# Performance work log

Measured on AMD Instinct MI355X. Metric: run time of the kernel, lower is better.

Reference implementation:

```python
import jax, jax.numpy as jnp
import numpy as np

N_NODES = 100000
N_EDGES = 4000000
CHANNELS = 64


def setup_inputs() -> dict:
    key = jax.random.key(0)
    k1, k2, k3, k4, k5 = jax.random.split(key, 5)
    x = jax.random.normal(k1, (N_NODES, CHANNELS), dtype=jnp.float32)
    sources = jax.random.randint(k2, (N_EDGES,), 0, N_NODES, dtype=jnp.int64)
    targets = jax.random.randint(k3, (N_EDGES,), 0, N_NODES, dtype=jnp.int64)
    norm = jax.random.uniform(k4, (N_NODES, 1), dtype=jnp.float32)
    # xavier_normal_ for a (64, 64) weight: std = sqrt(2 / (fan_in + fan_out))
    std = float(np.sqrt(2.0 / (CHANNELS + CHANNELS)))
    weight = jax.random.normal(k5, (CHANNELS, CHANNELS), dtype=jnp.float32) * std
    return {"x": x, "sources": sources, "targets": targets, "norm": norm, "weight": weight}


def reference(x, sources, targets, norm, weight):
    # x.index_add(0, targets, x[sources]) == x + segment_sum(x[sources], targets)
    messages = x[sources]  # [E, C] gather
    agg = x + jax.ops.segment_sum(messages, targets, num_segments=x.shape[0])  # [N, C]
    h = norm * agg  # per-node scale, norm broadcasts [N,1] over [N,C]
    return h @ weight  # [N, C]
```

## Files before the change

kernel.cpp:

```cpp
#include <hip/hip_runtime.h>


constexpr int C = 64;
constexpr int BN = 128;
constexpr int CHUNK2 = 8192;
constexpr int MAXB = 1024;
constexpr int NPASS = 3;
constexpr int BINS = BN * 4;
constexpr int ASTRIDE = 65;
constexpr int UNI = BN * ASTRIDE;
constexpr int TAILCAP = 65536;

__global__ __launch_bounds__(256) void init_kernel(
    int* __restrict__ cursor, int* __restrict__ tailcnt, int NB, int slot) {
  int i = blockIdx.x * 256 + threadIdx.x;
  if (i < NB) cursor[i] = i * slot;
  if (i == NB) *tailcnt = 0;
}

__global__ __launch_bounds__(512) void binfused_kernel(
    const int* __restrict__ src, const int* __restrict__ tgt,
    int* __restrict__ gcursor, int* __restrict__ tailcnt,
    unsigned* __restrict__ tailrec, unsigned* __restrict__ recs,
    const float* __restrict__ x, unsigned* __restrict__ xb,
    int E, int NB, int slot, int binBlocks, int total8) {
  if ((int)blockIdx.x >= binBlocks) {
    int i = (blockIdx.x - binBlocks) * 512 + threadIdx.x;
    if (i < total8) {
      const float4* x4 = (const float4*)x;
      float4 a = x4[i * 2], bq = x4[i * 2 + 1];
      float f[8] = {a.x, a.y, a.z, a.w, bq.x, bq.y, bq.z, bq.w};
      unsigned w[4];
#pragma unroll
      for (int k = 0; k < 4; k++) {
        unsigned u0 = __float_as_uint(f[2 * k]);
        unsigned u1 = __float_as_uint(f[2 * k + 1]);
        u0 = (u0 + 0x7FFFu + ((u0 >> 16) & 1u)) >> 16;
        u1 = (u1 + 0x7FFFu + ((u1 >> 16) & 1u)) >> 16;
        w[k] = u0 | (u1 << 16);
      }
      ((uint4*)xb)[i] = make_uint4(w[0], w[1], w[2], w[3]);
    }
    return;
  }
  __shared__ unsigned rec[CHUNK2];
  __shared__ unsigned short bkt[CHUNK2];
  __shared__ int hist[MAXB];
  __shared__ int gb[MAXB];
  int tid = threadIdx.x;
  int base = blockIdx.x * CHUNK2;
  int count = E - base; if (count > CHUNK2) count = CHUNK2;

  for (int i = tid; i < NB; i += 512) hist[i] = 0;
  __syncthreads();
  int nv = count >> 2;
  const int4* s4 = (const int4*)(src + base);
  const int4* t4 = (const int4*)(tgt + base);
  for (int i = tid; i < nv; i += 512) {
    int4 s = s4[i], t = t4[i];
    unsigned r0 = ((unsigned)s.x << 7) | (unsigned)(t.x & 127);
    unsigned r1 = ((unsigned)s.y << 7) | (unsigned)(t.y & 127);
    unsigned r2 = ((unsigned)s.z << 7) | (unsigned)(t.z & 127);
    unsigned r3 = ((unsigned)s.w << 7) | (unsigned)(t.w & 127);
    ((uint4*)rec)[i] = make_uint4(r0, r1, r2, r3);
    int b0 = t.x >> 7, b1 = t.y >> 7, b2 = t.z >> 7, b3 = t.w >> 7;
    ((ushort4*)bkt)[i] = make_ushort4(
        (unsigned short)b0, (unsigned short)b1,
        (unsigned short)b2, (unsigned short)b3);
    atomicAdd(&hist[b0], 1); atomicAdd(&hist[b1], 1);
    atomicAdd(&hist[b2], 1); atomicAdd(&hist[b3], 1);
  }
  for (int i = (nv << 2) + tid; i < count; i += 512) {
    int s = src[base + i], t = tgt[base + i];
    int b = t >> 7;
    rec[i] = ((unsigned)s << 7) | (unsigned)(t & 127);
    bkt[i] = (unsigned short)b;
    atomicAdd(&hist[b], 1);
  }
  __syncthreads();
  for (int i = tid; i < NB; i += 512) {
    int c = hist[i];
    gb[i] = c ? atomicAdd(&gcursor[i], c) : 0;
  }
  __syncthreads();
  for (int i = tid; i < NB; i += 512) hist[i] = 0;
  __syncthreads();
  for (int i = tid; i < count; i += 512) {
    int b = (int)bkt[i];
    int idx = atomicAdd(&hist[b], 1);
    int dest = gb[b] + idx;
    if (dest < (b + 1) * slot) {
      recs[dest] = rec[i];
    } else {
      int tp = atomicAdd(tailcnt, 1);
      if (tp < TAILCAP) {
        tailrec[2 * tp] = rec[i];
        tailrec[2 * tp + 1] = (unsigned)b;
      }
    }
  }
}

__device__ __forceinline__ void acc8_bf16(float (&a)[8], uint4 v) {
  a[0] += __uint_as_float(v.x << 16);
  a[1] += __uint_as_float(v.x & 0xFFFF0000u);
  a[2] += __uint_as_float(v.y << 16);
  a[3] += __uint_as_float(v.y & 0xFFFF0000u);
  a[4] += __uint_as_float(v.z << 16);
  a[5] += __uint_as_float(v.z & 0xFFFF0000u);
  a[6] += __uint_as_float(v.w << 16);
  a[7] += __uint_as_float(v.w & 0xFFFF0000u);
}

__device__ __forceinline__ void acc8_f32(float (&a)[8], float4 u, float4 v) {
  a[0] += u.x; a[1] += u.y; a[2] += u.z; a[3] += u.w;
  a[4] += v.x; a[5] += v.y; a[6] += v.z; a[7] += v.w;
}

template <bool USE_BF16>
__global__ __launch_bounds__(512, 2) void sortgather_kernel(
    const float* __restrict__ x, const unsigned* __restrict__ xb,
    const unsigned* __restrict__ recs, const int* __restrict__ cursor,
    const int* __restrict__ tailcnt, const unsigned* __restrict__ tailrec,
    const float* __restrict__ norm, const float* __restrict__ W,
    float* __restrict__ out, int N, int slot) {
  __shared__ int cnt[BINS];
  __shared__ int pre[BINS];
  __shared__ int nst[BINS + 1];
  __shared__ float uni[UNI];
  unsigned* sorted = (unsigned*)uni;
  float* accum = uni;
  int tid = threadIdx.x;
  int lane = tid & 63;
  int wave = tid >> 6;
  int b = blockIdx.x;
  int n0 = b * BN;
  int nn = N - n0; if (nn > BN) nn = BN;
  int beg = b * slot;
  int m = cursor[b] - beg; if (m > slot) m = slot;
  int end = beg + m;

  float wreg[C];
#pragma unroll
  for (int k = 0; k < C; k++) wreg[k] = W[k * C + lane];

  cnt[tid] = 0;
  __syncthreads();
  for (int r = beg + tid; r < end; r += 512) {
    unsigned rc = recs[r];
    int q = (int)(rc >> 22); if (q > 2) q = 2;
    atomicAdd(&cnt[(int)(rc & 127u) * 4 + q], 1);
  }
  __syncthreads();
  pre[tid] = cnt[tid];
  __syncthreads();
  for (int off = 1; off < BINS; off <<= 1) {
    int v = pre[tid];
    int a = (tid >= off) ? pre[tid - off] : 0;
    __syncthreads();
    pre[tid] = v + a;
    __syncthreads();
  }
  {
    int excl = pre[tid] - cnt[tid];
    nst[tid] = excl;
    cnt[tid] = excl;
  }
  if (tid == 0) nst[BINS] = m;
  __syncthreads();
  for (int r = beg + tid; r < end; r += 512) {
    unsigned rc = recs[r];
    int q = (int)(rc >> 22); if (q > 2) q = 2;
    int p = atomicAdd(&cnt[(int)(rc & 127u) * 4 + q], 1);
    sorted[p] = rc >> 7;
  }
  __syncthreads();

  int l7 = tid & 7;
  int g  = tid >> 3;
  int k0 = g, k1 = g + 64;
  bool has0 = k0 < nn, has1 = k1 < nn;
  const float4* x4 = (const float4*)x;
  const uint4* xb4 = (const uint4*)xb;

  float a0[8], a1[8];
  if (has0) {
    float4 u = x4[(n0 + k0) * 16 + l7 * 2], v = x4[(n0 + k0) * 16 + l7 * 2 + 1];
    a0[0] = u.x; a0[1] = u.y; a0[2] = u.z; a0[3] = u.w;
    a0[4] = v.x; a0[5] = v.y; a0[6] = v.z; a0[7] = v.w;
  } else {
#pragma unroll
    for (int j = 0; j < 8; j++) a0[j] = 0.0f;
  }
  if (has1) {
    float4 u = x4[(n0 + k1) * 16 + l7 * 2], v = x4[(n0 + k1) * 16 + l7 * 2 + 1];
    a1[0] = u.x; a1[1] = u.y; a1[2] = u.z; a1[3] = u.w;
    a1[4] = v.x; a1[5] = v.y; a1[6] = v.z; a1[7] = v.w;
  } else {
#pragma unroll
    for (int j = 0; j < 8; j++) a1[j] = 0.0f;
  }

#pragma unroll
  for (int p = 0; p < NPASS; p++) {
    if (has0) {
      int e = nst[k0 * 4 + p], ge = nst[k0 * 4 + p + 1];
      for (; e + 1 < ge; e += 2) {
        int s0 = (int)sorted[e], s1 = (int)sorted[e + 1];
        if (USE_BF16) {
          uint4 v0 = xb4[s0 * 8 + l7];
          uint4 v1 = xb4[s1 * 8 + l7];
          acc8_bf16(a0, v0); acc8_bf16(a0, v1);
        } else {
          float4 u0 = x4[s0 * 16 + l7 * 2], w0 = x4[s0 * 16 + l7 * 2 + 1];
          float4 u1 = x4[s1 * 16 + l7 * 2], w1 = x4[s1 * 16 + l7 * 2 + 1];
          acc8_f32(a0, u0, w0); acc8_f32(a0, u1, w1);
        }
      }
      if (e < ge) {
        int s = (int)sorted[e];
        if (USE_BF16) { uint4 v = xb4[s * 8 + l7]; acc8_bf16(a0, v); }
        else { acc8_f32(a0, x4[s * 16 + l7 * 2], x4[s * 16 + l7 * 2 + 1]); }
      }
    }
    if (has1) {
      int e = nst[k1 * 4 + p], ge = nst[k1 * 4 + p + 1];
      for (; e + 1 < ge; e += 2) {
        int s0 = (int)sorted[e], s1 = (int)sorted[e + 1];
        if (USE_BF16) {
          uint4 v0 = xb4[s0 * 8 + l7];
          uint4 v1 = xb4[s1 * 8 + l7];
          acc8_bf16(a1, v0); acc8_bf16(a1, v1);
        } else {
          float4 u0 = x4[s0 * 16 + l7 * 2], w0 = x4[s0 * 16 + l7 * 2 + 1];
          float4 u1 = x4[s1 * 16 + l7 * 2], w1 = x4[s1 * 16 + l7 * 2 + 1];
          acc8_f32(a1, u0, w0); acc8_f32(a1, u1, w1);
        }
      }
      if (e < ge) {
        int s = (int)sorted[e];
        if (USE_BF16) { uint4 v = xb4[s * 8 + l7]; acc8_bf16(a1, v); }
        else { acc8_f32(a1, x4[s * 16 + l7 * 2], x4[s * 16 + l7 * 2 + 1]); }
      }
    }
  }

  {
    int tc = *tailcnt; if (tc > TAILCAP) tc = TAILCAP;
    for (int r = 0; r < tc; r++) {
      if ((int)tailrec[2 * r + 1] != b) continue;
      unsigned rc = tailrec[2 * r];
      int tl = (int)(rc & 127u);
      if (tl == k0 || tl == k1) {
        int s = (int)(rc >> 7);
        if (USE_BF16) {
          uint4 v = xb4[s * 8 + l7];
          if (tl == k0) acc8_bf16(a0, v); else acc8_bf16(a1, v);
        } else {
          float4 u = x4[s * 16 + l7 * 2], w = x4[s * 16 + l7 * 2 + 1];
          if (tl == k0) acc8_f32(a0, u, w); else acc8_f32(a1, u, w);
        }
      }
    }
  }
  __syncthreads();

  if (has0) {
#pragma unroll
    for (int j = 0; j < 8; j++) accum[k0 * ASTRIDE + 8 * l7 + j] = a0[j];
  }
  if (has1) {
#pragma unroll
    for (int j = 0; j < 8; j++) accum[k1 * ASTRIDE + 8 * l7 + j] = a1[j];
  }
  __syncthreads();

  for (int i = wave; i < nn; i += 8) {
    int n = n0 + i;
    float a = accum[i * ASTRIDE + lane];
    float o = 0.0f;
#pragma unroll
    for (int c = 0; c < C; c++)
      o = fmaf(__shfl(a, c, 64), wreg[c], o);
    out[n * C + lane] = o * norm[n];
  }
}

extern "C" void kernel_launch(void* const* d_in, const int* in_sizes, int n_in,
                              void* d_out, int out_size, void* d_ws, size_t ws_size,
                              hipStream_t stream) {
  const float* x       = (const float*)d_in[0];
  const int*   sources = (const int*)d_in[1];
  const int*   targets = (const int*)d_in[2];
  const float* norm    = (const float*)d_in[3];
  const float* weight  = (const float*)d_in[4];
  float* out = (float*)d_out;

  int N = in_sizes[0] / C;
  int E = in_sizes[1];
  int NB = (N + BN - 1) / BN;

  size_t availw = ws_size / 4;
  size_t xw = (size_t)N * C / 2;
  size_t fixedw = (size_t)NB + 1 + 2 * (size_t)TAILCAP;
  bool use_bf16; int slot;
  if (availw >= xw + fixedw + (size_t)NB * 8192) { use_bf16 = true; slot = 8192; }
  else if (availw >= xw + fixedw + (size_t)NB * 6144) { use_bf16 = true; slot = 6144; }
  else {
    use_bf16 = false;
    size_t s = (availw > fixedw) ? (availw - fixedw) / (size_t)NB : 0;
    slot = s > 8192 ? 8192 : (int)s;
  }

  unsigned* xb; int* cursor;
  if (use_bf16) {
    xb = (unsigned*)d_ws;
    cursor = (int*)d_ws + xw;
  } else {
    xb = nullptr;
    cursor = (int*)d_ws;
  }
  int* tailcnt = cursor + NB;
  unsigned* tailrec = (unsigned*)(tailcnt + 1);
  unsigned* recs = tailrec + 2 * (size_t)TAILCAP;

  int hb = (E + CHUNK2 - 1) / CHUNK2;
  int total8 = N * C / 8;
  int cvtBlocks = use_bf16 ? (total8 + 511) / 512 : 0;

  init_kernel<<<(NB + 256) / 256, 256, 0, stream>>>(cursor, tailcnt, NB, slot);
  binfused_kernel<<<hb + cvtBlocks, 512, 0, stream>>>(
      sources, targets, cursor, tailcnt, tailrec, recs, x, xb,
      E, NB, slot, hb, total8);
  if (use_bf16) {
    sortgather_kernel<true><<<NB, 512, 0, stream>>>(
        x, xb, recs, cursor, tailcnt, tailrec, norm, weight, out, N, slot);
  } else {
    sortgather_kernel<false><<<NB, 512, 0, stream>>>(
        x, xb, recs, cursor, tailcnt, tailrec, norm, weight, out, N, slot);
  }
}
```

Baseline: 280.5 us.

## Refine source-range passes, cache records in registers, and single-pass binning offsets

In the binning kernel, the local offset returned by the histogram atomic is now kept with the bucket id, so the second atomic pass and the histogram reset go away. In the gather kernel, each thread loads its up to 16 records into registers once instead of reading global memory twice. Source-range sub-bins grow from 4 to 8 per target, giving finer locality across 7 passes; the scan handles two bins per thread. The W register load moves after sorting, the pass loop is no longer unrolled, and the occupancy hint rises to 6. Risks: register pressure from myrec plus wreg, and the code silently assumes at most 8192 records per bucket (slot).

Result: slower. 344.2 us (+22.7%).

```diff
diff --git a/kernel.cpp b/kernel.cpp
--- a/kernel.cpp
+++ b/kernel.cpp
@@ -5,8 +5,8 @@
 constexpr int BN = 128;
 constexpr int CHUNK2 = 8192;
 constexpr int MAXB = 1024;
-constexpr int NPASS = 3;
-constexpr int BINS = BN * 4;
+constexpr int NPASS = 7;
+constexpr int BINS = BN * 8;
 constexpr int ASTRIDE = 65;
 constexpr int UNI = BN * ASTRIDE;
 constexpr int TAILCAP = 65536;
@@ -44,7 +44,7 @@
     return;
   }
   __shared__ unsigned rec[CHUNK2];
-  __shared__ unsigned short bkt[CHUNK2];
+  __shared__ unsigned bi[CHUNK2];
   __shared__ int hist[MAXB];
   __shared__ int gb[MAXB];
   int tid = threadIdx.x;
@@ -64,18 +64,21 @@
     unsigned r3 = ((unsigned)s.w << 7) | (unsigned)(t.w & 127);
     ((uint4*)rec)[i] = make_uint4(r0, r1, r2, r3);
     int b0 = t.x >> 7, b1 = t.y >> 7, b2 = t.z >> 7, b3 = t.w >> 7;
-    ((ushort4*)bkt)[i] = make_ushort4(
-        (unsigned short)b0, (unsigned short)b1,
-        (unsigned short)b2, (unsigned short)b3);
-    atomicAdd(&hist[b0], 1); atomicAdd(&hist[b1], 1);
-    atomicAdd(&hist[b2], 1); atomicAdd(&hist[b3], 1);
+    unsigned i0 = (unsigned)atomicAdd(&hist[b0], 1);
+    unsigned i1 = (unsigned)atomicAdd(&hist[b1], 1);
+    unsigned i2 = (unsigned)atomicAdd(&hist[b2], 1);
+    unsigned i3 = (unsigned)atomicAdd(&hist[b3], 1);
+    ((uint4*)bi)[i] = make_uint4(((unsigned)b0 << 13) | i0,
+                                 ((unsigned)b1 << 13) | i1,
+                                 ((unsigned)b2 << 13) | i2,
+                                 ((unsigned)b3 << 13) | i3);
   }
   for (int i = (nv << 2) + tid; i < count; i += 512) {
     int s = src[base + i], t = tgt[base + i];
     int b = t >> 7;
     rec[i] = ((unsigned)s << 7) | (unsigned)(t & 127);
-    bkt[i] = (unsigned short)b;
-    atomicAdd(&hist[b], 1);
+    unsigned ix = (unsigned)atomicAdd(&hist[b], 1);
+    bi[i] = ((unsigned)b << 13) | ix;
   }
   __syncthreads();
   for (int i = tid; i < NB; i += 512) {
@@ -83,12 +86,10 @@
     gb[i] = c ? atomicAdd(&gcursor[i], c) : 0;
   }
   __syncthreads();
-  for (int i = tid; i < NB; i += 512) hist[i] = 0;
-  __syncthreads();
   for (int i = tid; i < count; i += 512) {
-    int b = (int)bkt[i];
-    int idx = atomicAdd(&hist[b], 1);
-    int dest = gb[b] + idx;
+    unsigned v = bi[i];
+    int b = (int)(v >> 13);
+    int dest = gb[b] + (int)(v & 8191u);
     if (dest < (b + 1) * slot) {
       recs[dest] = rec[i];
     } else {
@@ -118,14 +119,14 @@
 }
 
 template <bool USE_BF16>
-__global__ __launch_bounds__(512, 2) void sortgather_kernel(
+__global__ __launch_bounds__(512, 6) void sortgather_kernel(
     const float* __restrict__ x, const unsigned* __restrict__ xb,
     const unsigned* __restrict__ recs, const int* __restrict__ cursor,
     const int* __restrict__ tailcnt, const unsigned* __restrict__ tailrec,
     const float* __restrict__ norm, const float* __restrict__ W,
     float* __restrict__ out, int N, int slot) {
   __shared__ int cnt[BINS];
-  __shared__ int pre[BINS];
+  __shared__ int pre[512];
   __shared__ int nst[BINS + 1];
   __shared__ float uni[UNI];
   unsigned* sorted = (unsigned*)uni;
@@ -140,21 +141,27 @@
   int m = cursor[b] - beg; if (m > slot) m = slot;
   int end = beg + m;
 
-  float wreg[C];
-#pragma unroll
-  for (int k = 0; k < C; k++) wreg[k] = W[k * C + lane];
-
-  cnt[tid] = 0;
-  __syncthreads();
-  for (int r = beg + tid; r < end; r += 512) {
-    unsigned rc = recs[r];
-    int q = (int)(rc >> 22); if (q > 2) q = 2;
-    atomicAdd(&cnt[(int)(rc & 127u) * 4 + q], 1);
-  }
-  __syncthreads();
-  pre[tid] = cnt[tid];
-  __syncthreads();
-  for (int off = 1; off < BINS; off <<= 1) {
+  unsigned myrec[16];
+#pragma unroll
+  for (int j = 0; j < 16; j++) {
+    int r = beg + tid + j * 512;
+    myrec[j] = (r < end) ? recs[r] : 0xFFFFFFFFu;
+  }
+  cnt[tid] = 0; cnt[tid + 512] = 0;
+  __syncthreads();
+#pragma unroll
+  for (int j = 0; j < 16; j++) {
+    unsigned rc = myrec[j];
+    if (rc != 0xFFFFFFFFu) {
+      int q = (int)(rc >> 21); if (q > 6) q = 6;
+      atomicAdd(&cnt[((int)(rc & 127u) << 3) | q], 1);
+    }
+  }
+  __syncthreads();
+  int c0 = cnt[2 * tid], c1 = cnt[2 * tid + 1];
+  pre[tid] = c0 + c1;
+  __syncthreads();
+  for (int off = 1; off < 512; off <<= 1) {
     int v = pre[tid];
     int a = (tid >= off) ? pre[tid - off] : 0;
     __syncthreads();
@@ -162,19 +169,28 @@
     __syncthreads();
   }
   {
-    int excl = pre[tid] - cnt[tid];
-    nst[tid] = excl;
-    cnt[tid] = excl;
+    int run = pre[tid] - (c0 + c1);
+    nst[2 * tid] = run;
+    nst[2 * tid + 1] = run + c0;
+    cnt[2 * tid] = run;
+    cnt[2 * tid + 1] = run + c0;
   }
   if (tid == 0) nst[BINS] = m;
   __syncthreads();
-  for (int r = beg + tid; r < end; r += 512) {
-    unsigned rc = recs[r];
-    int q = (int)(rc >> 22); if (q > 2) q = 2;
-    int p = atomicAdd(&cnt[(int)(rc & 127u) * 4 + q], 1);
-    sorted[p] = rc >> 7;
-  }
-  __syncthreads();
+#pragma unroll
+  for (int j = 0; j < 16; j++) {
+    unsigned rc = myrec[j];
+    if (rc != 0xFFFFFFFFu) {
+      int q = (int)(rc >> 21); if (q > 6) q = 6;
+      int p = atomicAdd(&cnt[((int)(rc & 127u) << 3) | q], 1);
+      sorted[p] = rc >> 7;
+    }
+  }
+  __syncthreads();
+
+  float wreg[C];
+#pragma unroll
+  for (int k = 0; k < C; k++) wreg[k] = W[k * C + lane];
 
   int l7 = tid & 7;
   int g  = tid >> 3;
@@ -201,10 +217,9 @@
     for (int j = 0; j < 8; j++) a1[j] = 0.0f;
   }
 
-#pragma unroll
   for (int p = 0; p < NPASS; p++) {
     if (has0) {
-      int e = nst[k0 * 4 + p], ge = nst[k0 * 4 + p + 1];
+      int e = nst[k0 * 8 + p], ge = nst[k0 * 8 + p + 1];
       for (; e + 1 < ge; e += 2) {
         int s0 = (int)sorted[e], s1 = (int)sorted[e + 1];
         if (USE_BF16) {
@@ -224,7 +239,7 @@
       }
     }
     if (has1) {
-      int e = nst[k1 * 4 + p], ge = nst[k1 * 4 + p + 1];
+      int e = nst[k1 * 8 + p], ge = nst[k1 * 8 + p + 1];
       for (; e + 1 < ge; e += 2) {
         int s0 = (int)sorted[e], s1 = (int)sorted[e + 1];
         if (USE_BF16) {
```
